# Performance work log

Hardware: AMD Instinct MI355X
Metric: run time of the kernel (lower is better)

The kernel has to match this reference:

```python
import jax, jax.numpy as jnp
import numpy as np

N_NODES = 50000
N_EDGES = 1600000
IN_FEATS = 128
HID = 128
HEADS = 4
F_HEAD = HID // HEADS  # 32
NEG_SLOPE = 0.2


def setup_inputs() -> dict:
    key = jax.random.key(0)
    ks = jax.random.split(key, 7)
    feat = jax.random.normal(ks[0], (N_NODES, IN_FEATS), dtype=jnp.float32)
    # Xavier-ish scaling for the shared fc weight
    W = jax.random.normal(ks[1], (IN_FEATS, HID), dtype=jnp.float32) * (1.0 / np.sqrt(IN_FEATS))
    attn_l = jax.random.normal(ks[2], (HEADS, F_HEAD), dtype=jnp.float32) * 0.1
    attn_r = jax.random.normal(ks[3], (HEADS, F_HEAD), dtype=jnp.float32) * 0.1
    bias = jnp.zeros((HID,), dtype=jnp.float32)
    src_idx = jax.random.randint(ks[4], (N_EDGES,), 0, N_NODES, dtype=jnp.int32)
    dst_idx = jax.random.randint(ks[5], (N_EDGES,), 0, N_NODES, dtype=jnp.int32)
    return {"feat": feat, "W": W, "attn_l": attn_l, "attn_r": attn_r,
            "bias": bias, "src_idx": src_idx, "dst_idx": dst_idx}


def reference(feat, W, attn_l, attn_r, bias, src_idx, dst_idx):
    N = feat.shape[0]
    # shared linear projection, split into heads: [N, H, F]
    ft = (feat @ W).reshape(N, HEADS, F_HEAD)
    # per-node attention logits: [N, H]
    el = jnp.einsum('nhf,hf->nh', ft, attn_l)
    er = jnp.einsum('nhf,hf->nh', ft, attn_r)
    # per-edge unnormalized score: [E, H]
    e = jax.nn.leaky_relu(el[src_idx] + er[dst_idx], negative_slope=NEG_SLOPE)
    # numerically stable edge softmax grouped by destination node
    m = jax.ops.segment_max(e, dst_idx, num_segments=N)          # [N, H]
    m = jnp.where(jnp.isfinite(m), m, 0.0)                       # guard empty dst
    a = jnp.exp(e - m[dst_idx])                                  # [E, H]
    s = jax.ops.segment_sum(a, dst_idx, num_segments=N)          # [N, H]
    alpha = a / jnp.where(s[dst_idx] > 0, s[dst_idx], 1.0)       # [E, H]
    # weighted scatter-sum aggregation: [N, H, F]
    msgs = ft[src_idx] * alpha[:, :, None]
    out = jax.ops.segment_sum(msgs, dst_idx, num_segments=N)
    out = out + bias.reshape(1, HEADS, F_HEAD)
    return out.reshape(N, HEADS * F_HEAD)  # flatten(1)
```

## Files before the change

### kernel.cpp

```cpp
#include <hip/hip_runtime.h>
#include <hip/hip_bf16.h>
#include <math.h>

#define NEG_SLOPE 0.2f
#define NBMAX 1024
#define CAP_E 2560
#define CH 8192

typedef __attribute__((ext_vector_type(8))) short short8;
typedef __attribute__((ext_vector_type(4))) float f32x4;
typedef __attribute__((ext_vector_type(2))) float f32x2;
union BU { uint4 u; short8 s; };

__device__ __forceinline__ unsigned bf16rne(float f) {
    unsigned u = __float_as_uint(f);
    return (u + 0x7fffu + ((u >> 16) & 1u)) >> 16;
}
__device__ __forceinline__ short bf16s(float f) { return (short)bf16rne(f); }

__global__ __launch_bounds__(1024) void k_prepscat(
    const float* __restrict__ W, const float* __restrict__ attn_l,
    const float* __restrict__ attn_r, uint4* __restrict__ Wfrag,
    float4* __restrict__ WL, float4* __restrict__ WR,
    const int* __restrict__ src, const int* __restrict__ dst,
    int* __restrict__ gcur, unsigned* __restrict__ B, int E, int NB) {
    if (blockIdx.x < 3) {
        int gtid = blockIdx.x * 1024 + threadIdx.x;
        if (gtid < 2048) {
            int lane = gtid & 63;
            int ki = (gtid >> 6) & 3;
            int t = (gtid >> 8) & 3;
            int cg = gtid >> 10;
            int col = cg * 64 + t * 16 + (lane & 15);
            int kb = ki * 32 + (lane >> 4) * 8;
            unsigned d[4];
#pragma unroll
            for (int p = 0; p < 4; ++p) {
                unsigned lo = bf16rne(W[(kb + 2 * p) * 128 + col]);
                unsigned hi = bf16rne(W[(kb + 2 * p + 1) * 128 + col]);
                d[p] = lo | (hi << 16);
            }
            Wfrag[gtid] = make_uint4(d[0], d[1], d[2], d[3]);
        } else if (gtid < 2048 + 128) {
            int k = gtid - 2048;
            const float* wr_ = W + k * 128;
            float l0 = 0, l1 = 0, l2 = 0, l3 = 0, r0 = 0, r1 = 0, r2 = 0, r3 = 0;
            for (int j = 0; j < 32; ++j) {
                l0 += wr_[j] * attn_l[j];
                l1 += wr_[32 + j] * attn_l[32 + j];
                l2 += wr_[64 + j] * attn_l[64 + j];
                l3 += wr_[96 + j] * attn_l[96 + j];
                r0 += wr_[j] * attn_r[j];
                r1 += wr_[32 + j] * attn_r[32 + j];
                r2 += wr_[64 + j] * attn_r[64 + j];
                r3 += wr_[96 + j] * attn_r[96 + j];
            }
            WL[k] = make_float4(l0, l1, l2, l3);
            WR[k] = make_float4(r0, r1, r2, r3);
        }
        return;
    }
    __shared__ int h[NBMAX];
    __shared__ int lc[NBMAX];
    __shared__ int dl[CH];
    int tid = threadIdx.x;
    for (int t = tid; t < NB; t += 1024) h[t] = 0;
    __syncthreads();
    int beg = (blockIdx.x - 3) * CH;
    int end = min(beg + CH, E);
    for (int i = beg + tid; i < end; i += 1024) {
        int d = dst[i];
        dl[i - beg] = d;
        atomicAdd(&h[d >> 6], 1);
    }
    __syncthreads();
    for (int t = tid; t < NB; t += 1024)
        lc[t] = (h[t] > 0) ? atomicAdd(&gcur[t], h[t]) : 0;
    __syncthreads();
    for (int i = beg + tid; i < end; i += 1024) {
        int d = dl[i - beg];
        int pos = atomicAdd(&lc[d >> 6], 1);
        if (pos < CAP_E)
            B[(size_t)(d >> 6) * CAP_E + pos] = ((unsigned)src[i] << 6) | (unsigned)(d & 63);
    }
}

__global__ __launch_bounds__(256) void k_fc(
    const float* __restrict__ feat, const uint4* __restrict__ Wfrag,
    const f32x4* __restrict__ WL, const f32x4* __restrict__ WR,
    unsigned* __restrict__ ftbf, float* __restrict__ el, float* __restrict__ er,
    int N) {
    __shared__ f32x4 WLs[128], WRs[128];
    int tid = threadIdx.x;
    if (tid < 128) WLs[tid] = WL[tid];
    else WRs[tid - 128] = WR[tid - 128];
    __syncthreads();
    const int wave = tid >> 6, lane = tid & 63;
    const int rt = wave & 1, cg = wave >> 1;
    const int nbase = blockIdx.x * 32 + rt * 16;
    const int row = nbase + (lane & 15);
    const int rowc = min(row, N - 1);
    const int q = lane >> 4;

    BU b[4][4];
#pragma unroll
    for (int t = 0; t < 4; ++t)
#pragma unroll
        for (int ki = 0; ki < 4; ++ki)
            b[t][ki].u = Wfrag[cg * 1024 + t * 256 + ki * 64 + lane];

    f32x4 acc0 = {0, 0, 0, 0}, acc1 = {0, 0, 0, 0}, acc2 = {0, 0, 0, 0}, acc3 = {0, 0, 0, 0};
    f32x4 elacc = {0, 0, 0, 0}, eracc = {0, 0, 0, 0};
    const float* fr = feat + (size_t)rowc * 128;
#pragma unroll
    for (int ki = 0; ki < 4; ++ki) {
        float4 f0 = *(const float4*)(fr + ki * 32 + q * 8);
        float4 f1 = *(const float4*)(fr + ki * 32 + q * 8 + 4);
        short8 a;
        a[0] = bf16s(f0.x); a[1] = bf16s(f0.y); a[2] = bf16s(f0.z); a[3] = bf16s(f0.w);
        a[4] = bf16s(f1.x); a[5] = bf16s(f1.y); a[6] = bf16s(f1.z); a[7] = bf16s(f1.w);
        acc0 = __builtin_amdgcn_mfma_f32_16x16x32_bf16(a, b[0][ki].s, acc0, 0, 0, 0);
        acc1 = __builtin_amdgcn_mfma_f32_16x16x32_bf16(a, b[1][ki].s, acc1, 0, 0, 0);
        acc2 = __builtin_amdgcn_mfma_f32_16x16x32_bf16(a, b[2][ki].s, acc2, 0, 0, 0);
        acc3 = __builtin_amdgcn_mfma_f32_16x16x32_bf16(a, b[3][ki].s, acc3, 0, 0, 0);
        if (cg == 0) {
            int kb = ki * 32 + q * 8;
            elacc += f0.x * WLs[kb + 0]; eracc += f0.x * WRs[kb + 0];
            elacc += f0.y * WLs[kb + 1]; eracc += f0.y * WRs[kb + 1];
            elacc += f0.z * WLs[kb + 2]; eracc += f0.z * WRs[kb + 2];
            elacc += f0.w * WLs[kb + 3]; eracc += f0.w * WRs[kb + 3];
            elacc += f1.x * WLs[kb + 4]; eracc += f1.x * WRs[kb + 4];
            elacc += f1.y * WLs[kb + 5]; eracc += f1.y * WRs[kb + 5];
            elacc += f1.z * WLs[kb + 6]; eracc += f1.z * WRs[kb + 6];
            elacc += f1.w * WLs[kb + 7]; eracc += f1.w * WRs[kb + 7];
        }
    }
#pragma unroll
    for (int t = 0; t < 4; ++t) {
#pragma unroll
        for (int r = 0; r < 4; ++r) {
            float d = (t == 0) ? acc0[r] : (t == 1) ? acc1[r] : (t == 2) ? acc2[r] : acc3[r];
            unsigned m = bf16rne(d);
            unsigned nb = (unsigned)__shfl_xor((int)m, 1, 64);
            int node = nbase + q * 4 + r;
            int cp = cg * 32 + t * 8 + ((lane & 15) >> 1);
            if (!(lane & 1) && node < N)
                ftbf[(size_t)(cp >> 4) * ((size_t)N * 16) + (size_t)node * 16 + (cp & 15)]
                    = m | (nb << 16);
        }
    }
    if (cg == 0) {
#pragma unroll
        for (int c = 0; c < 4; ++c) {
            elacc[c] += __shfl_xor(elacc[c], 16, 64);
            eracc[c] += __shfl_xor(eracc[c], 16, 64);
            elacc[c] += __shfl_xor(elacc[c], 32, 64);
            eracc[c] += __shfl_xor(eracc[c], 32, 64);
        }
        if (lane < 16 && row < N) {
            *(float4*)(el + (size_t)row * 4) = make_float4(elacc[0], elacc[1], elacc[2], elacc[3]);
            *(float4*)(er + (size_t)row * 4) = make_float4(eracc[0], eracc[1], eracc[2], eracc[3]);
        }
    }
}

__global__ __launch_bounds__(512) void k_sort(
    const unsigned* __restrict__ B, const int* __restrict__ gcur,
    int* __restrict__ srt, uint2* __restrict__ od, int N) {
    __shared__ int hist[64];
    __shared__ int cur[64];
    const int tid = threadIdx.x;
    const int b = blockIdx.x;
    const int m = min(gcur[b], CAP_E);
    const size_t base = (size_t)b * CAP_E;
    if (tid < 64) hist[tid] = 0;
    __syncthreads();
    for (int i = tid; i < m; i += 512) atomicAdd(&hist[B[base + i] & 63], 1);
    __syncthreads();
    int v0 = (tid < 64) ? hist[tid] : 0;
    for (int off = 1; off < 64; off <<= 1) {
        int t = (tid < 64 && tid >= off) ? hist[tid - off] : 0;
        __syncthreads();
        if (tid < 64) hist[tid] += t;
        __syncthreads();
    }
    if (tid < 64) {
        int ex = hist[tid] - v0;
        cur[tid] = ex;
        int node = (b << 6) + tid;
        if (node < N) od[node] = make_uint2((unsigned)(base + ex), (unsigned)v0);
    }
    __syncthreads();
    for (int i = tid; i < m; i += 512) {
        unsigned p = B[base + i];
        int pos = atomicAdd(&cur[p & 63], 1);
        srt[base + pos] = (int)(p >> 6);
    }
}

__global__ __launch_bounds__(256, 8) void k_headpass(
    const unsigned* __restrict__ ftbf, const int* __restrict__ srt,
    const float* __restrict__ el, const float* __restrict__ er,
    const uint2* __restrict__ od, const float* __restrict__ bias,
    float* __restrict__ out, int N, int Nh) {
    const int d = blockIdx.x & 7;
    const int idx = blockIdx.x >> 3;
    const int h = d >> 1;
    const int half = d & 1;
    const int lane = threadIdx.x & 63;
    const int gl = lane & 15;
    const int es = gl >> 2;
    const int cq = gl & 3;
    const int node = half * Nh + idx * 16 + (threadIdx.x >> 6) * 4 + (lane >> 4);
    if (node >= N || node >= (half + 1) * Nh) return;
    uint2 o = od[node];
    const int* ah = srt + o.x;
    const int cnt = (int)o.y;
    const float erd = er[(size_t)node * 4 + h];
    const uint4* ftv = (const uint4*)(ftbf + (size_t)h * N * 16) + cq;

    float s = 0.f;
    f32x2 p0 = {0, 0}, p1 = {0, 0}, p2 = {0, 0}, p3 = {0, 0};
#pragma unroll 2
    for (int j = es; j < cnt; j += 4) {
        int sn = ah[j];
        float e = el[(size_t)sn * 4 + h] + erd;
        e = fmaxf(e, NEG_SLOPE * e);
        float a = __expf(e);
        uint4 u = ftv[(size_t)sn * 4];
        s += a;
        f32x2 a2 = {a, a};
        p0 += (f32x2){__uint_as_float(u.x << 16), __uint_as_float(u.x & 0xffff0000u)} * a2;
        p1 += (f32x2){__uint_as_float(u.y << 16), __uint_as_float(u.y & 0xffff0000u)} * a2;
        p2 += (f32x2){__uint_as_float(u.z << 16), __uint_as_float(u.z & 0xffff0000u)} * a2;
        p3 += (f32x2){__uint_as_float(u.w << 16), __uint_as_float(u.w & 0xffff0000u)} * a2;
    }
#pragma unroll
    for (int off2 = 4; off2 <= 8; off2 <<= 1) {
        p0.x += __shfl_xor(p0.x, off2, 64); p0.y += __shfl_xor(p0.y, off2, 64);
        p1.x += __shfl_xor(p1.x, off2, 64); p1.y += __shfl_xor(p1.y, off2, 64);
        p2.x += __shfl_xor(p2.x, off2, 64); p2.y += __shfl_xor(p2.y, off2, 64);
        p3.x += __shfl_xor(p3.x, off2, 64); p3.y += __shfl_xor(p3.y, off2, 64);
        s += __shfl_xor(s, off2, 64);
    }
    float inv = s > 0.f ? 1.f / s : 0.f;
    if (es == 0) {
        int c0 = h * 32 + cq * 8;
        float4 b0 = *(const float4*)(bias + c0);
        float4 b1 = *(const float4*)(bias + c0 + 4);
        float4 o0, o1;
        o0.x = p0.x * inv + b0.x; o0.y = p0.y * inv + b0.y;
        o0.z = p1.x * inv + b0.z; o0.w = p1.y * inv + b0.w;
        o1.x = p2.x * inv + b1.x; o1.y = p2.y * inv + b1.y;
        o1.z = p3.x * inv + b1.z; o1.w = p3.y * inv + b1.w;
        *(float4*)(out + (size_t)node * 128 + c0) = o0;
        *(float4*)(out + (size_t)node * 128 + c0 + 4) = o1;
    }
}

extern "C" void kernel_launch(void* const* d_in, const int* in_sizes, int n_in,
                              void* d_out, int out_size, void* d_ws, size_t ws_size,
                              hipStream_t stream) {
    const float* feat = (const float*)d_in[0];
    const float* W = (const float*)d_in[1];
    const float* attn_l = (const float*)d_in[2];
    const float* attn_r = (const float*)d_in[3];
    const float* bias = (const float*)d_in[4];
    const int* src = (const int*)d_in[5];
    const int* dst = (const int*)d_in[6];
    const int N = in_sizes[0] / 128;
    const int E = in_sizes[5];
    const int NB = (N + 63) >> 6;
    const int Nh = (N + 1) / 2;
    const int NBH = (Nh + 15) / 16;
    float* out = (float*)d_out;

    char* p = (char*)d_ws;
    unsigned int* ftbf = (unsigned int*)p;  p += (size_t)N * 64 * 4;
    unsigned* B = (unsigned*)p;             p += ((size_t)NB * CAP_E * 4 + 15) & ~15ull;
    int* srt = (int*)p;                     p += ((size_t)NB * CAP_E * 4 + 15) & ~15ull;
    float* el = (float*)p;                  p += (size_t)N * 4 * 4;
    float* er = (float*)p;                  p += (size_t)N * 4 * 4;
    uint2* od = (uint2*)p;                  p += (size_t)N * 8;
    int* gcur = (int*)p;                    p += ((size_t)NB * 4 + 15) & ~15ull;
    uint4* Wfrag = (uint4*)p;               p += 2048 * 16;
    float4* WL = (float4*)p;                p += 128 * 16;
    float4* WR = (float4*)p;                p += 128 * 16;

    int eblocks = (E + CH - 1) / CH;
    hipMemsetAsync(gcur, 0, (size_t)NB * 4, stream);
    k_prepscat<<<3 + eblocks, 1024, 0, stream>>>(W, attn_l, attn_r, Wfrag, WL, WR,
                                                 src, dst, gcur, B, E, NB);
    k_fc<<<(N + 31) / 32, 256, 0, stream>>>(feat, Wfrag, (const f32x4*)WL,
                                            (const f32x4*)WR, ftbf, el, er, N);
    k_sort<<<NB, 512, 0, stream>>>(B, gcur, srt, od, N);
    k_headpass<<<8 * NBH, 256, 0, stream>>>(ftbf, srt, el, er, od, bias, out, N, Nh);
}
```

Measured before the change: 126.6 us.

## Give each node a full wave in headpass and batch edge scores through LDS

The aggregation kernel now gives each destination node a whole 64-lane wave instead of 16 lanes. Each lane first computes one edge's attention weight, then the weights and source ids go through shared memory to a gather loop that covers 16 edges by 4 feature chunks per step. Source indices are stored as 16-bit values, and el is transposed to a per-head layout so the per-edge logit loads are contiguous. The aim is to cut the serial dependent-load chain per node and shrink index and logit traffic. In exchange, lanes sit idle for low-degree nodes and there are four times as many blocks. The 16-bit indices also assume fewer than 65536 nodes.

```diff
diff --git a/kernel.cpp b/kernel.cpp
--- a/kernel.cpp
+++ b/kernel.cpp
@@ -88,7 +88,7 @@
 __global__ __launch_bounds__(256) void k_fc(
     const float* __restrict__ feat, const uint4* __restrict__ Wfrag,
     const f32x4* __restrict__ WL, const f32x4* __restrict__ WR,
-    unsigned* __restrict__ ftbf, float* __restrict__ el, float* __restrict__ er,
+    unsigned* __restrict__ ftbf, float* __restrict__ el_t, float* __restrict__ er,
     int N) {
     __shared__ f32x4 WLs[128], WRs[128];
     int tid = threadIdx.x;
@@ -158,15 +158,18 @@
             eracc[c] += __shfl_xor(eracc[c], 32, 64);
         }
         if (lane < 16 && row < N) {
-            *(float4*)(el + (size_t)row * 4) = make_float4(elacc[0], elacc[1], elacc[2], elacc[3]);
             *(float4*)(er + (size_t)row * 4) = make_float4(eracc[0], eracc[1], eracc[2], eracc[3]);
+            el_t[row] = elacc[0];
+            el_t[(size_t)N + row] = elacc[1];
+            el_t[(size_t)2 * N + row] = elacc[2];
+            el_t[(size_t)3 * N + row] = elacc[3];
         }
     }
 }
 
 __global__ __launch_bounds__(512) void k_sort(
     const unsigned* __restrict__ B, const int* __restrict__ gcur,
-    int* __restrict__ srt, uint2* __restrict__ od, int N) {
+    unsigned short* __restrict__ srt16, uint2* __restrict__ od, int N) {
     __shared__ int hist[64];
     __shared__ int cur[64];
     const int tid = threadIdx.x;
@@ -194,58 +197,74 @@
     for (int i = tid; i < m; i += 512) {
         unsigned p = B[base + i];
         int pos = atomicAdd(&cur[p & 63], 1);
-        srt[base + pos] = (int)(p >> 6);
+        srt16[base + pos] = (unsigned short)(p >> 6);
     }
 }
 
 __global__ __launch_bounds__(256, 8) void k_headpass(
-    const unsigned* __restrict__ ftbf, const int* __restrict__ srt,
-    const float* __restrict__ el, const float* __restrict__ er,
+    const unsigned* __restrict__ ftbf, const unsigned short* __restrict__ srt16,
+    const float* __restrict__ el_t, const float* __restrict__ er,
     const uint2* __restrict__ od, const float* __restrict__ bias,
     float* __restrict__ out, int N, int Nh) {
+    __shared__ float als[4][64];
+    __shared__ unsigned snl[4][64];
     const int d = blockIdx.x & 7;
     const int idx = blockIdx.x >> 3;
     const int h = d >> 1;
     const int half = d & 1;
+    const int wave = threadIdx.x >> 6;
     const int lane = threadIdx.x & 63;
-    const int gl = lane & 15;
-    const int es = gl >> 2;
-    const int cq = gl & 3;
-    const int node = half * Nh + idx * 16 + (threadIdx.x >> 6) * 4 + (lane >> 4);
+    const int cq = lane & 3;
+    const int node = half * Nh + idx * 4 + wave;
     if (node >= N || node >= (half + 1) * Nh) return;
     uint2 o = od[node];
-    const int* ah = srt + o.x;
-    const int cnt = (int)o.y;
+    const int beg = (int)o.x, cnt = (int)o.y;
     const float erd = er[(size_t)node * 4 + h];
-    const uint4* ftv = (const uint4*)(ftbf + (size_t)h * N * 16) + cq;
+    const float* elh = el_t + (size_t)h * N;
+    const uint4* ftv = (const uint4*)(ftbf + (size_t)h * N * 16);
 
     float s = 0.f;
     f32x2 p0 = {0, 0}, p1 = {0, 0}, p2 = {0, 0}, p3 = {0, 0};
-#pragma unroll 2
-    for (int j = es; j < cnt; j += 4) {
-        int sn = ah[j];
-        float e = el[(size_t)sn * 4 + h] + erd;
-        e = fmaxf(e, NEG_SLOPE * e);
-        float a = __expf(e);
-        uint4 u = ftv[(size_t)sn * 4];
+    for (int tile = 0; tile < cnt; tile += 64) {
+        int tc = min(64, cnt - tile);
+        unsigned sn = 0;
+        float a = 0.f;
+        if (lane < tc) {
+            sn = srt16[beg + tile + lane];
+            float e = elh[sn] + erd;
+            e = fmaxf(e, NEG_SLOPE * e);
+            a = __expf(e);
+        }
         s += a;
-        f32x2 a2 = {a, a};
-        p0 += (f32x2){__uint_as_float(u.x << 16), __uint_as_float(u.x & 0xffff0000u)} * a2;
-        p1 += (f32x2){__uint_as_float(u.y << 16), __uint_as_float(u.y & 0xffff0000u)} * a2;
-        p2 += (f32x2){__uint_as_float(u.z << 16), __uint_as_float(u.z & 0xffff0000u)} * a2;
-        p3 += (f32x2){__uint_as_float(u.w << 16), __uint_as_float(u.w & 0xffff0000u)} * a2;
-    }
-#pragma unroll
-    for (int off2 = 4; off2 <= 8; off2 <<= 1) {
-        p0.x += __shfl_xor(p0.x, off2, 64); p0.y += __shfl_xor(p0.y, off2, 64);
-        p1.x += __shfl_xor(p1.x, off2, 64); p1.y += __shfl_xor(p1.y, off2, 64);
-        p2.x += __shfl_xor(p2.x, off2, 64); p2.y += __shfl_xor(p2.y, off2, 64);
-        p3.x += __shfl_xor(p3.x, off2, 64); p3.y += __shfl_xor(p3.y, off2, 64);
-        s += __shfl_xor(s, off2, 64);
+        als[wave][lane] = a;
+        snl[wave][lane] = sn;
+        for (int jj0 = 0; jj0 < tc; jj0 += 16) {
+            int j2 = jj0 + (lane >> 2);
+            int j3 = (j2 < tc) ? j2 : 0;
+            float af = als[wave][j3];
+            if (j2 >= tc) af = 0.f;
+            unsigned sn2 = snl[wave][j3];
+            uint4 u = ftv[(size_t)sn2 * 4 + cq];
+            f32x2 a2 = {af, af};
+            p0 += (f32x2){__uint_as_float(u.x << 16), __uint_as_float(u.x & 0xffff0000u)} * a2;
+            p1 += (f32x2){__uint_as_float(u.y << 16), __uint_as_float(u.y & 0xffff0000u)} * a2;
+            p2 += (f32x2){__uint_as_float(u.z << 16), __uint_as_float(u.z & 0xffff0000u)} * a2;
+            p3 += (f32x2){__uint_as_float(u.w << 16), __uint_as_float(u.w & 0xffff0000u)} * a2;
+        }
+    }
+    s += __shfl_xor(s, 1, 64);
+    s += __shfl_xor(s, 2, 64);
+#pragma unroll
+    for (int off = 4; off <= 32; off <<= 1) {
+        p0.x += __shfl_xor(p0.x, off, 64); p0.y += __shfl_xor(p0.y, off, 64);
+        p1.x += __shfl_xor(p1.x, off, 64); p1.y += __shfl_xor(p1.y, off, 64);
+        p2.x += __shfl_xor(p2.x, off, 64); p2.y += __shfl_xor(p2.y, off, 64);
+        p3.x += __shfl_xor(p3.x, off, 64); p3.y += __shfl_xor(p3.y, off, 64);
+        s += __shfl_xor(s, off, 64);
     }
     float inv = s > 0.f ? 1.f / s : 0.f;
-    if (es == 0) {
-        int c0 = h * 32 + cq * 8;
+    if (lane < 4) {
+        int c0 = h * 32 + lane * 8;
         float4 b0 = *(const float4*)(bias + c0);
         float4 b1 = *(const float4*)(bias + c0 + 4);
         float4 o0, o1;
@@ -272,14 +291,14 @@
     const int E = in_sizes[5];
     const int NB = (N + 63) >> 6;
     const int Nh = (N + 1) / 2;
-    const int NBH = (Nh + 15) / 16;
+    const int NBH = (Nh + 3) / 4;
     float* out = (float*)d_out;
 
     char* p = (char*)d_ws;
     unsigned int* ftbf = (unsigned int*)p;  p += (size_t)N * 64 * 4;
     unsigned* B = (unsigned*)p;             p += ((size_t)NB * CAP_E * 4 + 15) & ~15ull;
-    int* srt = (int*)p;                     p += ((size_t)NB * CAP_E * 4 + 15) & ~15ull;
-    float* el = (float*)p;                  p += (size_t)N * 4 * 4;
+    unsigned short* srt16 = (unsigned short*)p; p += ((size_t)NB * CAP_E * 2 + 15) & ~15ull;
+    float* el_t = (float*)p;                p += (size_t)N * 4 * 4;
     float* er = (float*)p;                  p += (size_t)N * 4 * 4;
     uint2* od = (uint2*)p;                  p += (size_t)N * 8;
     int* gcur = (int*)p;                    p += ((size_t)NB * 4 + 15) & ~15ull;
@@ -292,7 +311,7 @@
     k_prepscat<<<3 + eblocks, 1024, 0, stream>>>(W, attn_l, attn_r, Wfrag, WL, WR,
                                                  src, dst, gcur, B, E, NB);
     k_fc<<<(N + 31) / 32, 256, 0, stream>>>(feat, Wfrag, (const f32x4*)WL,
-                                            (const f32x4*)WR, ftbf, el, er, N);
-    k_sort<<<NB, 512, 0, stream>>>(B, gcur, srt, od, N);
-    k_headpass<<<8 * NBH, 256, 0, stream>>>(ftbf, srt, el, er, od, bias, out, N, Nh);
-}
+                                            (const f32x4*)WR, ftbf, el_t, er, N);
+    k_sort<<<NB, 512, 0, stream>>>(B, gcur, srt16, od, N);
+    k_headpass<<<8 * NBH, 256, 0, stream>>>(ftbf, srt16, el_t, er, od, bias, out, N, Nh);
+}
```

After: 149.9 us. 18.4% more time.
